# Kernel optimization log

Measured on AMD Instinct MI355X. Metric: run time of the kernel, lower is better.

Reference implementation:

```python
import jax, jax.numpy as jnp
import numpy as np

INPUT_DIM = 1024
HIDDEN_DIM = 1024

def setup_inputs() -> dict:
    key = jax.random.key(0)
    ks = jax.random.split(key, 9)
    s_in = 1.0 / np.sqrt(INPUT_DIM)
    s_h = 1.0 / np.sqrt(HIDDEN_DIM)
    x = jax.random.normal(ks[0], (4, 2048, INPUT_DIM), dtype=jnp.float32)
    Wq = jax.random.uniform(ks[1], (INPUT_DIM, HIDDEN_DIM), jnp.float32, -s_in, s_in)
    bq = jax.random.uniform(ks[2], (HIDDEN_DIM,), jnp.float32, -s_in, s_in)
    Wk = jax.random.uniform(ks[3], (INPUT_DIM, HIDDEN_DIM), jnp.float32, -s_in, s_in)
    bk = jax.random.uniform(ks[4], (HIDDEN_DIM,), jnp.float32, -s_in, s_in)
    Wv = jax.random.uniform(ks[5], (INPUT_DIM, HIDDEN_DIM), jnp.float32, -s_in, s_in)
    bv = jax.random.uniform(ks[6], (HIDDEN_DIM,), jnp.float32, -s_in, s_in)
    Wo = jax.random.uniform(ks[7], (HIDDEN_DIM, INPUT_DIM), jnp.float32, -s_h, s_h)
    bo = jax.random.uniform(ks[8], (INPUT_DIM,), jnp.float32, -s_h, s_h)
    return {"x": x, "Wq": Wq, "bq": bq, "Wk": Wk, "bk": bk, "Wv": Wv, "bv": bv, "Wo": Wo, "bo": bo}

def reference(x, Wq, bq, Wk, bk, Wv, bv, Wo, bo):
    # x: [B, S, D_in]; scale uses x.shape[-1] (faithful to source, which divides by sqrt(input_dim))
    scale = 1.0 / jnp.sqrt(jnp.asarray(x.shape[-1], dtype=x.dtype))
    Q = jnp.einsum('bsd,dh->bsh', x, Wq) + bq
    K = jnp.einsum('bsd,dh->bsh', x, Wk) + bk
    V = jnp.einsum('bsd,dh->bsh', x, Wv) + bv
    scores = jnp.einsum('bqh,bkh->bqk', Q, K) * scale  # [B, S, S]
    attn = jax.nn.softmax(scores, axis=-1)
    ctx = jnp.einsum('bqk,bkh->bqh', attn, V)
    return jnp.einsum('bsh,hd->bsd', ctx, Wo) + bo
```

## Files before the change

kernel.cpp:

```cpp
#include <hip/hip_runtime.h>

typedef __attribute__((ext_vector_type(8))) short bf16x8;
typedef __attribute__((ext_vector_type(4))) float f32x4;
typedef __attribute__((ext_vector_type(4))) unsigned short us4;

#define AS1 __attribute__((address_space(1)))
#define AS3 __attribute__((address_space(3)))

__device__ __forceinline__ unsigned short f2bf(float f) {
  unsigned u = __float_as_uint(f);
  u += 0x7fff + ((u >> 16) & 1);
  return (unsigned short)(u >> 16);
}

__device__ __forceinline__ void gload_lds16(const void* g, void* l) {
  __builtin_amdgcn_global_load_lds((const AS1 unsigned int*)g,
                                   (AS3 unsigned int*)l, 16, 0, 0);
}

#define MFMA16(a, b, c) __builtin_amdgcn_mfma_f32_16x16x32_bf16(a, b, c, 0, 0, 0)

template <typename OutT, bool BIAS, int MODE, int BM>
__global__ __launch_bounds__(2 * BM, (BM == 256) ? 2 : 3) void gemmk(
    const unsigned short* __restrict__ A,
    const unsigned short* __restrict__ Bt,
    OutT* __restrict__ C,
    unsigned short* __restrict__ Vt,
    const float* __restrict__ bias,
    int Kd, int lda, int ldb, int ldc,
    long sA, long sB, long sC,
    float scale) {
  constexpr int THREADS = 2 * BM;
  constexpr int ABUF  = BM * 32;
  constexpr int BUFSZ = ABUF + 128 * 32;
  __shared__ unsigned short lds[3 * BUFSZ];

  const int bz = blockIdx.z;
  A  += (size_t)bz * sA + (size_t)blockIdx.x * BM * lda;
  Bt += (size_t)bz * sB + (size_t)blockIdx.y * 128 * ldb;

  const int tid  = threadIdx.x;
  const int wave = tid >> 6;
  const int lane = tid & 63;
  const int wm   = wave >> 1;
  const int wn   = wave & 1;
  const int l15  = lane & 15;
  const int hi   = lane >> 4;
  const int srow = tid >> 2;
  const int schk = ((tid & 3) ^ ((tid >> 3) & 3)) * 8;

  auto stage = [&](int bi, int k0) {
    unsigned short* L = &lds[bi * BUFSZ + wave * 512];
    const unsigned short* ga = A + (size_t)srow * lda + (k0 + schk);
    const unsigned short* gb = Bt + (size_t)srow * ldb + (k0 + schk);
    if constexpr (BM == 256) {
      gload_lds16(ga, L);
      gload_lds16(ga + (size_t)128 * lda, L + 4096);
      gload_lds16(gb, L + ABUF);
    } else {
      gload_lds16(ga, L);
      gload_lds16(ga + (size_t)64 * lda, L + 2048);
      gload_lds16(gb, L + ABUF);
      gload_lds16(gb + (size_t)64 * ldb, L + ABUF + 2048);
    }
  };

  f32x4 acc[4][4] = {};

  stage(0, 0);
  stage(1, 32);
  if constexpr (BM == 256) asm volatile("s_waitcnt vmcnt(3)" ::: "memory");
  else                     asm volatile("s_waitcnt vmcnt(4)" ::: "memory");
  __builtin_amdgcn_s_barrier();

  const int NT = Kd >> 5;
  int bufi = 0;
  const int xh  = (hi ^ ((l15 >> 1) & 3)) * 8;
  const int rdA = (wm * 64 + l15) * 32 + xh;
  const int rdB = ABUF + (wn * 64 + l15) * 32 + xh;
  for (int t = 0; t < NT; ++t) {
    if (t + 2 < NT) {
      int nbi = bufi + 2; if (nbi >= 3) nbi -= 3;
      stage(nbi, (t + 2) << 5);
    }
    const unsigned short* L = &lds[bufi * BUFSZ];
    bf16x8 af[4], bf[4];
#pragma unroll
    for (int mt = 0; mt < 4; ++mt)
      af[mt] = *(const bf16x8*)&L[rdA + mt * 512];
#pragma unroll
    for (int nt = 0; nt < 4; ++nt)
      bf[nt] = *(const bf16x8*)&L[rdB + nt * 512];
    __builtin_amdgcn_s_setprio(1);
#pragma unroll
    for (int mt = 0; mt < 4; ++mt)
#pragma unroll
      for (int nt = 0; nt < 4; ++nt)
        acc[mt][nt] = MFMA16(af[mt], bf[nt], acc[mt][nt]);
    __builtin_amdgcn_s_setprio(0);
    if (t + 2 < NT) {
      if constexpr (BM == 256) asm volatile("s_waitcnt vmcnt(3)" ::: "memory");
      else                     asm volatile("s_waitcnt vmcnt(4)" ::: "memory");
    } else if (t + 1 < NT) {
      asm volatile("s_waitcnt vmcnt(0)" ::: "memory");
    }
    __builtin_amdgcn_s_barrier();
    bufi = (bufi + 1 == 3) ? 0 : bufi + 1;
  }

  const int hi4  = hi << 2;
  const int row0 = blockIdx.x * BM + wm * 64;
  const int col0 = blockIdx.y * 128 + wn * 64;

  if constexpr (MODE == 1) {
    const int piece = col0 >> 10;
    float bvv[4];
#pragma unroll
    for (int nt = 0; nt < 4; ++nt)
      bvv[nt] = BIAS ? bias[col0 + nt * 16 + l15] : 0.0f;
    if (piece < 2) {
      OutT* dst = C + (size_t)piece * sC;
      const int cb = (col0 & 1023) + l15;
#pragma unroll
      for (int mt = 0; mt < 4; ++mt)
#pragma unroll
        for (int r = 0; r < 4; ++r) {
          const size_t rowoff = (size_t)(row0 + mt * 16 + hi4 + r) * ldc;
#pragma unroll
          for (int nt = 0; nt < 4; ++nt)
            dst[rowoff + cb + nt * 16] = (OutT)f2bf(acc[mt][nt][r] * scale + bvv[nt]);
        }
    } else {
      const int b = blockIdx.x >> 3;
      const int sb = (blockIdx.x & 7) * 256 + wm * 64 + hi4;
#pragma unroll
      for (int nt = 0; nt < 4; ++nt) {
        const int d = ((col0 + nt * 16) & 1023) + l15;
#pragma unroll
        for (int mt = 0; mt < 4; ++mt) {
          us4 pk;
          pk.x = f2bf(acc[mt][nt][0] * scale + bvv[nt]);
          pk.y = f2bf(acc[mt][nt][1] * scale + bvv[nt]);
          pk.z = f2bf(acc[mt][nt][2] * scale + bvv[nt]);
          pk.w = f2bf(acc[mt][nt][3] * scale + bvv[nt]);
          *(us4*)&Vt[((size_t)b << 21) + (size_t)d * 2048 + sb + mt * 16] = pk;
        }
      }
    }
  } else {
    C += (size_t)bz * sC;
    float bvv[4];
#pragma unroll
    for (int nt = 0; nt < 4; ++nt)
      bvv[nt] = BIAS ? bias[col0 + nt * 16 + l15] : 0.0f;
    const int cb = col0 + l15;
#pragma unroll
    for (int mt = 0; mt < 4; ++mt)
#pragma unroll
      for (int r = 0; r < 4; ++r) {
        const size_t rowoff = (size_t)(row0 + mt * 16 + hi4 + r) * ldc;
#pragma unroll
        for (int nt = 0; nt < 4; ++nt) {
          const float v = acc[mt][nt][r] * scale + bvv[nt];
          if constexpr (sizeof(OutT) == 4)
            C[rowoff + cb + nt * 16] = v;
          else
            C[rowoff + cb + nt * 16] = (OutT)f2bf(v);
        }
      }
  }
}

__global__ void cvt_x(const float* __restrict__ in, unsigned short* __restrict__ out, int n4) {
  const int i = blockIdx.x * blockDim.x + threadIdx.x;
  if (i < n4) {
    const float4 v = ((const float4*)in)[i];
    uint2 o;
    o.x = (unsigned)f2bf(v.x) | ((unsigned)f2bf(v.y) << 16);
    o.y = (unsigned)f2bf(v.z) | ((unsigned)f2bf(v.w) << 16);
    ((uint2*)out)[i] = o;
  }
}

__global__ void cvtT_w4(const float* __restrict__ Wq, const float* __restrict__ Wk,
                        const float* __restrict__ Wv, const float* __restrict__ Wo,
                        unsigned short* __restrict__ Wqkvb, unsigned short* __restrict__ Wob) {
  __shared__ unsigned short tile[64][65];
  const int z = blockIdx.z;
  const float* in = (z == 0) ? Wq : (z == 1) ? Wk : (z == 2) ? Wv : Wo;
  unsigned short* out = (z == 3) ? Wob : Wqkvb + (size_t)z * 1024 * 1024;
  const int r0 = blockIdx.y * 64, c0 = blockIdx.x * 64;
  for (int i = threadIdx.y; i < 64; i += 4)
    tile[i][threadIdx.x] = f2bf(in[(size_t)(r0 + i) * 1024 + c0 + threadIdx.x]);
  __syncthreads();
  for (int i = threadIdx.y; i < 64; i += 4)
    out[(size_t)(c0 + i) * 1024 + r0 + threadIdx.x] = tile[threadIdx.x][i];
}

__global__ void concat_bias(const float* __restrict__ bq, const float* __restrict__ bk,
                            const float* __restrict__ bv, float* __restrict__ dst) {
  const int z = blockIdx.x;
  const float* src = (z == 0) ? bq : (z == 1) ? bk : bv;
  const int i = threadIdx.x;
  ((float4*)(dst + z * 1024))[i] = ((const float4*)src)[i];
}

__global__ __launch_bounds__(512) void softmax_w(unsigned short* __restrict__ scores) {
  const int lane = threadIdx.x & 63;
  unsigned short* p =
      scores + ((size_t)blockIdx.x * 8 + (threadIdx.x >> 6)) * 2048;
  uint4 raw[4];
  float v[32];
#pragma unroll
  for (int g = 0; g < 4; ++g) raw[g] = ((const uint4*)p)[lane + g * 64];
#pragma unroll
  for (int g = 0; g < 4; ++g) {
    v[g * 8 + 0] = __uint_as_float(raw[g].x << 16);
    v[g * 8 + 1] = __uint_as_float(raw[g].x & 0xffff0000u);
    v[g * 8 + 2] = __uint_as_float(raw[g].y << 16);
    v[g * 8 + 3] = __uint_as_float(raw[g].y & 0xffff0000u);
    v[g * 8 + 4] = __uint_as_float(raw[g].z << 16);
    v[g * 8 + 5] = __uint_as_float(raw[g].z & 0xffff0000u);
    v[g * 8 + 6] = __uint_as_float(raw[g].w << 16);
    v[g * 8 + 7] = __uint_as_float(raw[g].w & 0xffff0000u);
  }
  float m = v[0];
#pragma unroll
  for (int i = 1; i < 32; ++i) m = fmaxf(m, v[i]);
#pragma unroll
  for (int off = 32; off; off >>= 1) m = fmaxf(m, __shfl_xor(m, off, 64));
  float s = 0.f;
#pragma unroll
  for (int i = 0; i < 32; ++i) { v[i] = __expf(v[i] - m); s += v[i]; }
#pragma unroll
  for (int off = 32; off; off >>= 1) s += __shfl_xor(s, off, 64);
  const float inv = 1.0f / s;
#pragma unroll
  for (int g = 0; g < 4; ++g) {
    uint4 ov;
    ov.x = (unsigned)f2bf(v[g * 8 + 0] * inv) | ((unsigned)f2bf(v[g * 8 + 1] * inv) << 16);
    ov.y = (unsigned)f2bf(v[g * 8 + 2] * inv) | ((unsigned)f2bf(v[g * 8 + 3] * inv) << 16);
    ov.z = (unsigned)f2bf(v[g * 8 + 4] * inv) | ((unsigned)f2bf(v[g * 8 + 5] * inv) << 16);
    ov.w = (unsigned)f2bf(v[g * 8 + 6] * inv) | ((unsigned)f2bf(v[g * 8 + 7] * inv) << 16);
    ((uint4*)p)[lane + g * 64] = ov;
  }
}

extern "C" void kernel_launch(void* const* d_in, const int* in_sizes, int n_in,
                              void* d_out, int out_size, void* d_ws, size_t ws_size,
                              hipStream_t stream) {
  const float* x  = (const float*)d_in[0];
  const float* Wq = (const float*)d_in[1];
  const float* bq = (const float*)d_in[2];
  const float* Wk = (const float*)d_in[3];
  const float* bk = (const float*)d_in[4];
  const float* Wv = (const float*)d_in[5];
  const float* bv = (const float*)d_in[6];
  const float* Wo = (const float*)d_in[7];
  const float* bo = (const float*)d_in[8];
  float* out = (float*)d_out;

  char* ws = (char*)d_ws;
  size_t off = 0;
  auto alloc = [&](size_t bytes) { char* p = ws + off; off += (bytes + 255) & ~255UL; return p; };
  unsigned short* xb    = (unsigned short*)alloc(8192UL * 1024 * 2);
  unsigned short* Wqkvb = (unsigned short*)alloc(3072UL * 1024 * 2);
  unsigned short* Wob   = (unsigned short*)alloc(1024UL * 1024 * 2);
  float*          bqkv  = (float*)alloc(3072UL * 4);
  unsigned short* Qb    = (unsigned short*)alloc(8192UL * 1024 * 2);
  unsigned short* Kb    = (unsigned short*)alloc(8192UL * 1024 * 2);
  unsigned short* Vtb   = (unsigned short*)alloc(4UL * 1024 * 2048 * 2);
  unsigned short* attn  = (unsigned short*)alloc(8192UL * 2048 * 2);
  unsigned short* ctxb  = (unsigned short*)alloc(8192UL * 1024 * 2);

  cvt_x<<<2097152 / 256, 256, 0, stream>>>(x, xb, 2097152);
  cvtT_w4<<<dim3(16, 16, 4), dim3(64, 4), 0, stream>>>(Wq, Wk, Wv, Wo, Wqkvb, Wob);
  concat_bias<<<3, 256, 0, stream>>>(bq, bk, bv, bqkv);

  gemmk<unsigned short, true, 1, 256><<<dim3(32, 24, 1), 512, 0, stream>>>(
      xb, Wqkvb, Qb, Vtb, bqkv, 1024, 1024, 1024, 1024, 0, 0, 8192L * 1024, 1.0f);

  gemmk<unsigned short, false, 0, 256><<<dim3(8, 16, 4), 512, 0, stream>>>(
      Qb, Kb, attn, nullptr, nullptr, 1024, 1024, 1024, 2048,
      2048L * 1024, 2048L * 1024, 2048L * 2048, 0.03125f);

  softmax_w<<<1024, 512, 0, stream>>>(attn);

  gemmk<unsigned short, false, 0, 128><<<dim3(16, 8, 4), 256, 0, stream>>>(
      attn, Vtb, ctxb, nullptr, nullptr, 2048, 2048, 2048, 1024,
      2048L * 2048, 1024L * 2048, 2048L * 1024, 1.0f);

  gemmk<float, true, 0, 128><<<dim3(64, 8, 1), 256, 0, stream>>>(
      ctxb, Wob, out, nullptr, bo, 1024, 1024, 1024, 1024, 0, 0, 0, 1.0f);
}
```

Before: 280.9 us.

## Add 256x256-tile 8-wave GEMM with ping-pong LDS schedule for QKV and scores

```diff
diff --git a/kernel.cpp b/kernel.cpp
--- a/kernel.cpp
+++ b/kernel.cpp
@@ -19,9 +19,12 @@
 }
 
 #define MFMA16(a, b, c) __builtin_amdgcn_mfma_f32_16x16x32_bf16(a, b, c, 0, 0, 0)
-
-template <typename OutT, bool BIAS, int MODE, int BM>
-__global__ __launch_bounds__(2 * BM, (BM == 256) ? 2 : 3) void gemmk(
+#define BARRIER() __builtin_amdgcn_s_barrier()
+#define LGKM0() asm volatile("s_waitcnt lgkmcnt(0)" ::: "memory")
+#define VMCNT(n) asm volatile("s_waitcnt vmcnt(" #n ")" ::: "memory")
+
+template <typename OutT, bool BIAS, int MODE>
+__global__ __launch_bounds__(512, 2) void gemm8(
     const unsigned short* __restrict__ A,
     const unsigned short* __restrict__ Bt,
     OutT* __restrict__ C,
@@ -30,13 +33,206 @@
     int Kd, int lda, int ldb, int ldc,
     long sA, long sB, long sC,
     float scale) {
-  constexpr int THREADS = 2 * BM;
-  constexpr int ABUF  = BM * 32;
+  constexpr int BBASE = 256 * 64;
+  constexpr int BUF0 = 0, BUF1 = 2 * BBASE;
+  __shared__ unsigned short lds[4 * BBASE];
+
+  const int bz = blockIdx.z;
+  A  += (size_t)bz * sA + (size_t)blockIdx.x * 256 * lda;
+  Bt += (size_t)bz * sB + (size_t)blockIdx.y * 256 * ldb;
+
+  const int tid  = threadIdx.x;
+  const int wave = tid >> 6;
+  const int lane = tid & 63;
+  const int wm   = wave >> 2;
+  const int wn   = wave & 3;
+  const int l15  = lane & 15;
+  const int hi   = lane >> 4;
+  const int srow = tid >> 3;
+  const int schk = ((tid & 7) ^ ((tid >> 3) & 7)) * 8;
+  int aoff[2], boff[2];
+#pragma unroll
+  for (int ks = 0; ks < 2; ++ks) {
+    const int slot = ((ks * 4 + hi) ^ (l15 & 7)) * 8;
+    aoff[ks] = (wm * 128 + l15) * 64 + slot;
+    boff[ks] = BBASE + ((wn >> 1) * 64 + (wn & 1) * 32 + l15) * 64 + slot;
+  }
+
+  auto stA = [&](int buf, int r0, int k0) {
+    const unsigned short* g = A + (size_t)(r0 + srow) * lda + (k0 + schk);
+    gload_lds16(g, &lds[buf + r0 * 64 + wave * 512]);
+  };
+  auto stB = [&](int buf, int lr0, int k0) {
+    const int lr = lr0 + srow;
+    const int gc = ((lr >> 6) & 1) * 128 + ((lr >> 5) & 1) * 64 +
+                   (lr >> 7) * 32 + (lr & 31);
+    const unsigned short* g = Bt + (size_t)gc * ldb + (k0 + schk);
+    gload_lds16(g, &lds[buf + BBASE + lr0 * 64 + wave * 512]);
+  };
+
+  f32x4 acc[8][4] = {};
+  bf16x8 af[4][2], bf0[2][2], bf1[2][2];
+
+  auto dsA = [&](int buf, int mq) {
+#pragma unroll
+    for (int mf = 0; mf < 4; ++mf)
+#pragma unroll
+      for (int ks = 0; ks < 2; ++ks)
+        af[mf][ks] = *(const bf16x8*)&lds[buf + (mq * 64 + mf * 16) * 64 + aoff[ks]];
+  };
+  auto dsB = [&](bf16x8 (&bf)[2][2], int buf, int nq) {
+#pragma unroll
+    for (int nf = 0; nf < 2; ++nf)
+#pragma unroll
+      for (int ks = 0; ks < 2; ++ks)
+        bf[nf][ks] = *(const bf16x8*)&lds[buf + nq * 8192 + nf * 1024 + boff[ks]];
+  };
+  auto mmq = [&](bf16x8 (&bf)[2][2], int mq, int nq) {
+#pragma unroll
+    for (int mf = 0; mf < 4; ++mf)
+#pragma unroll
+      for (int nf = 0; nf < 2; ++nf) {
+        f32x4* a = &acc[mq * 4 + mf][nq * 2 + nf];
+        *a = MFMA16(af[mf][0], bf[nf][0], *a);
+        *a = MFMA16(af[mf][1], bf[nf][1], *a);
+      }
+  };
+
+  stA(BUF0, 0, 0);    stA(BUF0, 128, 0);
+  stB(BUF0, 0, 0);    stB(BUF0, 64, 0);
+  stB(BUF0, 128, 0);  stB(BUF0, 192, 0);
+  stA(BUF0, 64, 0);   stA(BUF0, 192, 0);
+  stA(BUF1, 0, 64);   stA(BUF1, 128, 64);
+  stB(BUF1, 128, 64); stB(BUF1, 192, 64);
+  VMCNT(0);
+  BARRIER();
+
+  const int NP = Kd >> 7;
+  for (int j = 0; j < NP; ++j) {
+    const int k1 = ((2 * j + 1) << 6);
+    const int k2 = k1 + 64, k3 = k1 + 128;
+    const bool st = (j + 1) < NP;
+
+    dsA(BUF0, 0); dsB(bf0, BUF0, 0);
+    stA(BUF1, 64, k1); stA(BUF1, 192, k1);
+    BARRIER(); LGKM0();
+    __builtin_amdgcn_s_setprio(1); mmq(bf0, 0, 0); __builtin_amdgcn_s_setprio(0);
+    BARRIER();
+    dsB(bf1, BUF0, 1);
+    stB(BUF1, 0, k1); stB(BUF1, 64, k1);
+    BARRIER(); LGKM0();
+    __builtin_amdgcn_s_setprio(1); mmq(bf1, 0, 1); __builtin_amdgcn_s_setprio(0);
+    BARRIER();
+    dsA(BUF0, 1);
+    if (st) { stA(BUF0, 0, k2); stA(BUF0, 128, k2); }
+    BARRIER(); LGKM0();
+    __builtin_amdgcn_s_setprio(1); mmq(bf1, 1, 1); __builtin_amdgcn_s_setprio(0);
+    BARRIER();
+    if (st) { stB(BUF0, 128, k2); stB(BUF0, 192, k2); }
+    BARRIER(); LGKM0();
+    __builtin_amdgcn_s_setprio(1); mmq(bf0, 1, 0); __builtin_amdgcn_s_setprio(0);
+    if (st) { VMCNT(4); } else { VMCNT(0); }
+    BARRIER();
+    dsA(BUF1, 0); dsB(bf0, BUF1, 0);
+    if (st) { stA(BUF0, 64, k2); stA(BUF0, 192, k2); }
+    BARRIER(); LGKM0();
+    __builtin_amdgcn_s_setprio(1); mmq(bf0, 0, 0); __builtin_amdgcn_s_setprio(0);
+    BARRIER();
+    dsB(bf1, BUF1, 1);
+    if (st) { stB(BUF0, 0, k2); stB(BUF0, 64, k2); }
+    BARRIER(); LGKM0();
+    __builtin_amdgcn_s_setprio(1); mmq(bf1, 0, 1); __builtin_amdgcn_s_setprio(0);
+    BARRIER();
+    dsA(BUF1, 1);
+    if (st) { stA(BUF1, 0, k3); stA(BUF1, 128, k3); }
+    BARRIER(); LGKM0();
+    __builtin_amdgcn_s_setprio(1); mmq(bf1, 1, 1); __builtin_amdgcn_s_setprio(0);
+    BARRIER();
+    if (st) { stB(BUF1, 128, k3); stB(BUF1, 192, k3); }
+    BARRIER(); LGKM0();
+    __builtin_amdgcn_s_setprio(1); mmq(bf0, 1, 0); __builtin_amdgcn_s_setprio(0);
+    if (st) { VMCNT(4); }
+    BARRIER();
+  }
+
+  const int hi4  = hi << 2;
+  const int row0 = blockIdx.x * 256 + wm * 128;
+  const int col0 = blockIdx.y * 256 + wn * 64;
+
+  if constexpr (MODE == 1) {
+    const int piece = col0 >> 10;
+    float bvv[4];
+#pragma unroll
+    for (int nt = 0; nt < 4; ++nt)
+      bvv[nt] = BIAS ? bias[col0 + nt * 16 + l15] : 0.0f;
+    if (piece < 2) {
+      OutT* dst = C + (size_t)piece * sC;
+      const int cb = (col0 & 1023) + l15;
+#pragma unroll
+      for (int mt = 0; mt < 8; ++mt)
+#pragma unroll
+        for (int r = 0; r < 4; ++r) {
+          const size_t rowoff = (size_t)(row0 + mt * 16 + hi4 + r) * ldc;
+#pragma unroll
+          for (int nt = 0; nt < 4; ++nt)
+            dst[rowoff + cb + nt * 16] = (OutT)f2bf(acc[mt][nt][r] * scale + bvv[nt]);
+        }
+    } else {
+      const int b = blockIdx.x >> 3;
+      const int sb = (blockIdx.x & 7) * 256 + wm * 128 + hi4;
+#pragma unroll
+      for (int nt = 0; nt < 4; ++nt) {
+        const int d = ((col0 + nt * 16) & 1023) + l15;
+#pragma unroll
+        for (int mt = 0; mt < 8; ++mt) {
+          us4 pk;
+          pk.x = f2bf(acc[mt][nt][0] * scale + bvv[nt]);
+          pk.y = f2bf(acc[mt][nt][1] * scale + bvv[nt]);
+          pk.z = f2bf(acc[mt][nt][2] * scale + bvv[nt]);
+          pk.w = f2bf(acc[mt][nt][3] * scale + bvv[nt]);
+          *(us4*)&Vt[((size_t)b << 21) + (size_t)d * 2048 + sb + mt * 16] = pk;
+        }
+      }
+    }
+  } else {
+    C += (size_t)bz * sC;
+    float bvv[4];
+#pragma unroll
+    for (int nt = 0; nt < 4; ++nt)
+      bvv[nt] = BIAS ? bias[col0 + nt * 16 + l15] : 0.0f;
+    const int cb = col0 + l15;
+#pragma unroll
+    for (int mt = 0; mt < 8; ++mt)
+#pragma unroll
+      for (int r = 0; r < 4; ++r) {
+        const size_t rowoff = (size_t)(row0 + mt * 16 + hi4 + r) * ldc;
+#pragma unroll
+        for (int nt = 0; nt < 4; ++nt) {
+          const float v = acc[mt][nt][r] * scale + bvv[nt];
+          if constexpr (sizeof(OutT) == 4)
+            C[rowoff + cb + nt * 16] = v;
+          else
+            C[rowoff + cb + nt * 16] = (OutT)f2bf(v);
+        }
+      }
+  }
+}
+
+template <typename OutT, bool BIAS>
+__global__ __launch_bounds__(256, 3) void gemmk(
+    const unsigned short* __restrict__ A,
+    const unsigned short* __restrict__ Bt,
+    OutT* __restrict__ C,
+    const float* __restrict__ bias,
+    int Kd, int lda, int ldb, int ldc,
+    long sA, long sB, long sC,
+    float scale) {
+  constexpr int ABUF  = 128 * 32;
   constexpr int BUFSZ = ABUF + 128 * 32;
   __shared__ unsigned short lds[3 * BUFSZ];
 
   const int bz = blockIdx.z;
-  A  += (size_t)bz * sA + (size_t)blockIdx.x * BM * lda;
+  A  += (size_t)bz * sA + (size_t)blockIdx.x * 128 * lda;
   Bt += (size_t)bz * sB + (size_t)blockIdx.y * 128 * ldb;
 
   const int tid  = threadIdx.x;
@@ -52,26 +248,18 @@
   auto stage = [&](int bi, int k0) {
     unsigned short* L = &lds[bi * BUFSZ + wave * 512];
     const unsigned short* ga = A + (size_t)srow * lda + (k0 + schk);
+    gload_lds16(ga, L);
+    gload_lds16(ga + (size_t)64 * lda, L + 2048);
     const unsigned short* gb = Bt + (size_t)srow * ldb + (k0 + schk);
-    if constexpr (BM == 256) {
-      gload_lds16(ga, L);
-      gload_lds16(ga + (size_t)128 * lda, L + 4096);
-      gload_lds16(gb, L + ABUF);
-    } else {
-      gload_lds16(ga, L);
-      gload_lds16(ga + (size_t)64 * lda, L + 2048);
-      gload_lds16(gb, L + ABUF);
-      gload_lds16(gb + (size_t)64 * ldb, L + ABUF + 2048);
-    }
+    gload_lds16(gb, L + ABUF);
+    gload_lds16(gb + (size_t)64 * ldb, L + ABUF + 2048);
   };
 
   f32x4 acc[4][4] = {};
-
   stage(0, 0);
   stage(1, 32);
-  if constexpr (BM == 256) asm volatile("s_waitcnt vmcnt(3)" ::: "memory");
-  else                     asm volatile("s_waitcnt vmcnt(4)" ::: "memory");
-  __builtin_amdgcn_s_barrier();
+  VMCNT(4);
+  BARRIER();
 
   const int NT = Kd >> 5;
   int bufi = 0;
@@ -98,77 +286,35 @@
       for (int nt = 0; nt < 4; ++nt)
         acc[mt][nt] = MFMA16(af[mt], bf[nt], acc[mt][nt]);
     __builtin_amdgcn_s_setprio(0);
-    if (t + 2 < NT) {
-      if constexpr (BM == 256) asm volatile("s_waitcnt vmcnt(3)" ::: "memory");
-      else                     asm volatile("s_waitcnt vmcnt(4)" ::: "memory");
-    } else if (t + 1 < NT) {
-      asm volatile("s_waitcnt vmcnt(0)" ::: "memory");
-    }
-    __builtin_amdgcn_s_barrier();
+    if (t + 2 < NT)      { VMCNT(4); }
+    else if (t + 1 < NT) { VMCNT(0); }
+    BARRIER();
     bufi = (bufi + 1 == 3) ? 0 : bufi + 1;
   }
 
   const int hi4  = hi << 2;
-  const int row0 = blockIdx.x * BM + wm * 64;
+  const int row0 = blockIdx.x * 128 + wm * 64;
   const int col0 = blockIdx.y * 128 + wn * 64;
-
-  if constexpr (MODE == 1) {
-    const int piece = col0 >> 10;
-    float bvv[4];
-#pragma unroll
-    for (int nt = 0; nt < 4; ++nt)
-      bvv[nt] = BIAS ? bias[col0 + nt * 16 + l15] : 0.0f;
-    if (piece < 2) {
-      OutT* dst = C + (size_t)piece * sC;
-      const int cb = (col0 & 1023) + l15;
-#pragma unroll
-      for (int mt = 0; mt < 4; ++mt)
-#pragma unroll
-        for (int r = 0; r < 4; ++r) {
-          const size_t rowoff = (size_t)(row0 + mt * 16 + hi4 + r) * ldc;
-#pragma unroll
-          for (int nt = 0; nt < 4; ++nt)
-            dst[rowoff + cb + nt * 16] = (OutT)f2bf(acc[mt][nt][r] * scale + bvv[nt]);
-        }
-    } else {
-      const int b = blockIdx.x >> 3;
-      const int sb = (blockIdx.x & 7) * 256 + wm * 64 + hi4;
+  C += (size_t)bz * sC;
+  float bvv[4];
+#pragma unroll
+  for (int nt = 0; nt < 4; ++nt)
+    bvv[nt] = BIAS ? bias[col0 + nt * 16 + l15] : 0.0f;
+  const int cb = col0 + l15;
+#pragma unroll
+  for (int mt = 0; mt < 4; ++mt)
+#pragma unroll
+    for (int r = 0; r < 4; ++r) {
+      const size_t rowoff = (size_t)(row0 + mt * 16 + hi4 + r) * ldc;
 #pragma unroll
       for (int nt = 0; nt < 4; ++nt) {
-        const int d = ((col0 + nt * 16) & 1023) + l15;
-#pragma unroll
-        for (int mt = 0; mt < 4; ++mt) {
-          us4 pk;
-          pk.x = f2bf(acc[mt][nt][0] * scale + bvv[nt]);
-          pk.y = f2bf(acc[mt][nt][1] * scale + bvv[nt]);
-          pk.z = f2bf(acc[mt][nt][2] * scale + bvv[nt]);
-          pk.w = f2bf(acc[mt][nt][3] * scale + bvv[nt]);
-          *(us4*)&Vt[((size_t)b << 21) + (size_t)d * 2048 + sb + mt * 16] = pk;
-        }
+        const float v = acc[mt][nt][r] * scale + bvv[nt];
+        if constexpr (sizeof(OutT) == 4)
+          C[rowoff + cb + nt * 16] = v;
+        else
+          C[rowoff + cb + nt * 16] = (OutT)f2bf(v);
       }
     }
-  } else {
-    C += (size_t)bz * sC;
-    float bvv[4];
-#pragma unroll
-    for (int nt = 0; nt < 4; ++nt)
-      bvv[nt] = BIAS ? bias[col0 + nt * 16 + l15] : 0.0f;
-    const int cb = col0 + l15;
-#pragma unroll
-    for (int mt = 0; mt < 4; ++mt)
-#pragma unroll
-      for (int r = 0; r < 4; ++r) {
-        const size_t rowoff = (size_t)(row0 + mt * 16 + hi4 + r) * ldc;
-#pragma unroll
-        for (int nt = 0; nt < 4; ++nt) {
-          const float v = acc[mt][nt][r] * scale + bvv[nt];
-          if constexpr (sizeof(OutT) == 4)
-            C[rowoff + cb + nt * 16] = v;
-          else
-            C[rowoff + cb + nt * 16] = (OutT)f2bf(v);
-        }
-      }
-  }
 }
 
 __global__ void cvt_x(const float* __restrict__ in, unsigned short* __restrict__ out, int n4) {
@@ -277,19 +423,19 @@
   cvtT_w4<<<dim3(16, 16, 4), dim3(64, 4), 0, stream>>>(Wq, Wk, Wv, Wo, Wqkvb, Wob);
   concat_bias<<<3, 256, 0, stream>>>(bq, bk, bv, bqkv);
 
-  gemmk<unsigned short, true, 1, 256><<<dim3(32, 24, 1), 512, 0, stream>>>(
+  gemm8<unsigned short, true, 1><<<dim3(32, 12, 1), 512, 0, stream>>>(
       xb, Wqkvb, Qb, Vtb, bqkv, 1024, 1024, 1024, 1024, 0, 0, 8192L * 1024, 1.0f);
 
-  gemmk<unsigned short, false, 0, 256><<<dim3(8, 16, 4), 512, 0, stream>>>(
+  gemm8<unsigned short, false, 0><<<dim3(8, 8, 4), 512, 0, stream>>>(
       Qb, Kb, attn, nullptr, nullptr, 1024, 1024, 1024, 2048,
       2048L * 1024, 2048L * 1024, 2048L * 2048, 0.03125f);
 
   softmax_w<<<1024, 512, 0, stream>>>(attn);
 
-  gemmk<unsigned short, false, 0, 128><<<dim3(16, 8, 4), 256, 0, stream>>>(
-      attn, Vtb, ctxb, nullptr, nullptr, 2048, 2048, 2048, 1024,
+  gemmk<unsigned short, false><<<dim3(16, 8, 4), 256, 0, stream>>>(
+      attn, Vtb, ctxb, nullptr, 2048, 2048, 2048, 1024,
       2048L * 2048, 1024L * 2048, 2048L * 1024, 1.0f);
 
-  gemmk<float, true, 0, 128><<<dim3(64, 8, 1), 256, 0, stream>>>(
-      ctxb, Wob, out, nullptr, bo, 1024, 1024, 1024, 1024, 0, 0, 0, 1.0f);
-}
+  gemmk<float, true><<<dim3(64, 8, 1), 256, 0, stream>>>(
+      ctxb, Wob, out, bo, 1024, 1024, 1024, 1024, 0, 0, 0, 1.0f);
+}
```

Result: slower. 292.1 us (+4.0%).
